# Performance work log

Hardware: AMD Instinct MI355X
Metric: run time of the kernel (lower is better)

Reference implementation:

```python
import jax, jax.numpy as jnp
import numpy as np

# MyConvT config (matches init_kwargs)
K, S, P, OP = 5, 2, 2, 1  # kernel, stride, padding, output_padding


def setup_inputs() -> dict:
    key = jax.random.key(0)
    k0, k1, k2, k3 = jax.random.split(key, 4)
    B, Cin, Cout, H, W = 8, 192, 128, 64, 64
    OH = (H - 1) * S + K - 2 * P + OP  # 128
    OW = (W - 1) * S + K - 2 * P + OP  # 128
    x = jax.random.normal(k0, (B, Cin, H, W), jnp.float32)
    # mask spatial must be (OH + K - 1, OW + K - 1) so its unfold has OH*OW columns
    mask = jax.random.randint(k1, (B, 1, OH + K - 1, OW + K - 1), 0, 2, jnp.int32)
    # torch ConvTranspose2d weight layout: [in_channels, out_channels, kH, kW]
    weight = jax.random.normal(k2, (Cin, Cout, K, K), jnp.float32) * 0.05
    bias = jax.random.normal(k3, (Cout,), jnp.float32) * 0.05
    return {"x": x, "mask": mask, "weight": weight, "bias": bias}


def _masked_conv_transpose(x, mask, weight, bias):
    # The torch module does: zero-insert (stride dilation), pad (K-1-P each side,
    # plus OP trailing), unfold, gather valid patches (where the unfolded mask
    # patch has any nonzero), dense matmul with rot180/transposed weight + bias,
    # then masked_scatter back (zeros elsewhere). Mathematically:
    #   out = mask_any * (conv_transpose2d(x, weight) + bias)
    # where mask_any[b,oh,ow] = any(mask[b,:, oh:oh+K, ow:ow+K] != 0).
    kern = jnp.flip(weight, (2, 3)).transpose(1, 0, 2, 3)  # -> OIHW correlation kernel
    pad = ((K - 1 - P, K - 1 - P + OP), (K - 1 - P, K - 1 - P + OP))
    y = jax.lax.conv_general_dilated(
        x, kern, window_strides=(1, 1), padding=pad, lhs_dilation=(S, S),
        dimension_numbers=("NCHW", "OIHW", "NCHW"))  # [B, Cout, OH, OW]
    m = (mask != 0).astype(y.dtype)  # [B, 1, OH+K-1, OW+K-1]
    pooled = jax.lax.reduce_window(m, 0.0, jax.lax.max,
                                   (1, 1, K, K), (1, 1, 1, 1), "VALID")  # [B,1,OH,OW]
    return jnp.where(pooled > 0, y + bias[None, :, None, None], 0.0)


def reference(x, mask, weight, bias):
    return _masked_conv_transpose(x, mask, weight, bias)
```

## Files before the change

kernel.cpp:

```cpp
#include <hip/hip_runtime.h>


#define NB   8
#define CIN  192
#define COUT 128
#define HH   64
#define OHH  128
#define OWW  128
#define MH   132
#define MW   132

#define X4_IYH_B 27648
#define PLANE_B  9216
#define XBUF_B   36864
#define WOFF     36864
#define NSLOT    5
#define LDS_B    (XBUF_B + NSLOT * 8192)

typedef short bf16x8 __attribute__((ext_vector_type(8)));
typedef float f32x4  __attribute__((ext_vector_type(4)));
typedef float f32x2  __attribute__((ext_vector_type(2)));

static __device__ __forceinline__ unsigned short f2bf(float f) {
  union { float f; unsigned int u; } a; a.f = f;
  return (unsigned short)((a.u + 0x7fffu + ((a.u >> 16) & 1u)) >> 16);
}

#define GLOAD_LDS16(gp, lp) __builtin_amdgcn_global_load_lds(                      \
    (const __attribute__((address_space(1))) void*)(gp),                           \
    (__attribute__((address_space(3))) void*)(lp), 16, 0, 0)

__global__ __launch_bounds__(256) void prep_k(
    const float* __restrict__ x, const int* __restrict__ mask,
    const float* __restrict__ w, unsigned short* __restrict__ x4,
    unsigned short* __restrict__ w4, unsigned char* __restrict__ many) {
  const int bid = blockIdx.x, tid = threadIdx.x;

  if (bid < 528) {
    const int b = bid / 66, iyH = bid % 66;
    const int lane = tid & 63, wv = tid >> 6;
    unsigned short* pl = x4 + (size_t)(b * 66 + iyH) * (X4_IYH_B / 2);

    if (iyH == 0 || iyH == 65) {
      for (int i = tid; i < X4_IYH_B / 16; i += 256)
        *(uint4*)(pl + i * 8) = make_uint4(0, 0, 0, 0);
      return;
    }
    const int iy = iyH - 1;
    if (tid < 48) {
      int c3 = tid >> 4, rr = (tid >> 3) & 1, ch = tid & 7;
      *(uint4*)(pl + (c3 * 72 + rr * 65) * 64 + ch * 8) = make_uint4(0, 0, 0, 0);
    }
    #pragma unroll
    for (int k = 0; k < 6; ++k) {
      int ci0 = wv * 48 + k * 8;
      int c3 = ci0 >> 6, cr = ci0 & 63;
      unsigned short p[8];
      #pragma unroll
      for (int e = 0; e < 8; ++e)
        p[e] = f2bf(x[(((size_t)b * CIN + ci0 + e) * HH + iy) * HH + lane]);
      uint4 v;
      v.x = (unsigned)p[0] | ((unsigned)p[1] << 16);
      v.y = (unsigned)p[2] | ((unsigned)p[3] << 16);
      v.z = (unsigned)p[4] | ((unsigned)p[5] << 16);
      v.w = (unsigned)p[6] | ((unsigned)p[7] << 16);
      *(uint4*)(pl + ((size_t)c3 * 72 + 1 + lane) * 64 + cr) = v;
    }
  } else if (bid < 624) {
    int idx = (bid - 528) * 256 + tid;
    int ci = idx % CIN, co = idx / CIN;
    int cob = co >> 6, c = co & 63, c3 = ci >> 6, cir = ci & 63;
    const float* src = w + (size_t)(ci * COUT + co) * 25;
    #pragma unroll
    for (int tap = 0; tap < 25; ++tap)
      w4[(size_t)((tap * 2 + cob) * 3 + c3) * 4096 + c * 64 + cir] = f2bf(src[tap]);
  } else {
    int g = (bid - 624) * 256 + tid;
    int owq = g & 31, oh = (g >> 5) & 127, b = g >> 12;
    const int* mp = mask + (b * MH + oh) * MW + owq * 4;
    int a0 = 0, a1 = 0, a2 = 0, a3 = 0;
    #pragma unroll
    for (int i = 0; i < 5; ++i) {
      int4 u = *(const int4*)(mp + i * MW);
      int4 v = *(const int4*)(mp + i * MW + 4);
      int c = u.z | u.w | v.x;
      a0 |= u.x | u.y | c;
      a1 |= u.y | c | v.y;
      a2 |= c | v.y | v.z;
      a3 |= u.w | v.x | v.y | v.z | v.w;
    }
    *(uchar4*)(many + ((size_t)b * OHH + oh) * OWW + owq * 4) =
        make_uchar4(a0 ? 1 : 0, a1 ? 1 : 0, a2 ? 1 : 0, a3 ? 1 : 0);
  }
}


#define VMC(N) asm volatile("s_waitcnt vmcnt(" #N ")" ::: "memory")

#define GATE(T)                                                                \
  { if ((T) == 24 && c3 == 2)      VMC(0);                                     \
    else if ((T) == 22 && c3 == 2) VMC(2);                                     \
    else                           VMC(6);                                     \
    __builtin_amdgcn_s_barrier(); }

#define BF_LOAD(KK, KJ)                                                        \
  { const int p_ = oyr + 2 - (KK);                                             \
    _Pragma("unroll") for (int k2 = 0; k2 < 2; ++k2)                           \
      _Pragma("unroll") for (int ti = 0; ti < 4; ++ti) {                       \
        const int row_ = ti * 16 + l15 + 2 - (KJ);                             \
        bfr[k2][ti] = *(const bf16x8*)(lds + p_ * PLANE_B + row_ * 128 +       \
                                       (((k2 * 4 + kc) ^ (row_ & 7)) << 4)); } }

#define AF_LOADJ(J, T)                                                         \
  { const char* ws_ = lds + WOFF + ((T) % 5) * 8192;                           \
    _Pragma("unroll") for (int k2 = 0; k2 < 2; ++k2)                           \
      _Pragma("unroll") for (int mi = 0; mi < 2; ++mi) {                       \
        const int row_ = cos * 32 + mi * 16 + l15;                             \
        afr[J][k2][mi] = *(const bf16x8*)(ws_ + row_ * 128 +                   \
                                          (((k2 * 4 + kc) ^ (l15 & 7)) << 4)); } }

#define MMJ(J, PH_, PW_)                                                       \
  { __builtin_amdgcn_s_setprio(1);                                             \
    _Pragma("unroll") for (int k2 = 0; k2 < 2; ++k2)                           \
      _Pragma("unroll") for (int mi = 0; mi < 2; ++mi)                         \
        _Pragma("unroll") for (int ti = 0; ti < 4; ++ti)                       \
          acc[PH_][PW_][mi][ti] = __builtin_amdgcn_mfma_f32_16x16x32_bf16(     \
              afr[J][k2][mi], bfr[k2][ti], acc[PH_][PW_][mi][ti], 0, 0, 0);    \
    __builtin_amdgcn_s_setprio(0); }

#define PAIRB(T, KK, KJ, PH0, PW0, PH1, PW1)                                   \
  { stage_u((T) + 3); stage_u((T) + 4); GATE(T)                                \
    BF_LOAD(KK, KJ) AF_LOADJ(0, T) AF_LOADJ(1, (T) + 1)                        \
    MMJ(0, PH0, PW0) MMJ(1, PH1, PW1) }
#define PAIRN(T, PH0, PW0, PH1, PW1)                                           \
  { stage_u((T) + 3); stage_u((T) + 4); GATE(T)                                \
    AF_LOADJ(0, T) AF_LOADJ(1, (T) + 1)                                        \
    MMJ(0, PH0, PW0) MMJ(1, PH1, PW1) }
#define PH1B(T, KK, KJ, PH0, PW0)                                              \
  { stage_u((T) + 3); GATE(T)                                                  \
    BF_LOAD(KK, KJ) AF_LOADJ(0, T) MMJ(0, PH0, PW0) }

__global__ __launch_bounds__(256, 2) void convt_mfma(
    const unsigned short* __restrict__ x4, const unsigned short* __restrict__ w4,
    const float* __restrict__ bias, const unsigned char* __restrict__ many,
    float* __restrict__ out) {
  __shared__ __align__(16) char lds[LDS_B];
  constexpr int TID[25] = {0,1,5,6, 2,3,7,8, 4,9, 10,11,15,16, 12,13,17,18,
                           14,19, 20,21, 22,23, 24};

  const int tid = threadIdx.x, lane = tid & 63, wv = tid >> 6;
  const int l15 = lane & 15, kc = lane >> 4;
  const int cos = wv & 1, oyr = wv >> 1;
  const int b = blockIdx.x & 7, qq = blockIdx.x >> 3;
  const int cob = qq & 1, oyq = qq >> 1;
  const int oy0 = oyq * 2, oy = oy0 + oyr;
  const int sswz = (lane >> 3) * 128 + (((lane & 7) ^ (lane >> 3)) << 4);

  const char* x4b = (const char*)x4 + (size_t)(b * 66 + oy0) * X4_IYH_B;
  const char* w4b = (const char*)w4 + cob * 24576;

  f32x4 acc[2][2][2][4];
  #pragma unroll
  for (int p = 0; p < 2; ++p)
    #pragma unroll
    for (int q2 = 0; q2 < 2; ++q2)
      #pragma unroll
      for (int i = 0; i < 2; ++i)
        #pragma unroll
        for (int j = 0; j < 4; ++j)
          acc[p][q2][i][j] = (f32x4){0.f, 0.f, 0.f, 0.f};

  auto stage_x = [&](int c3) {
    #pragma unroll
    for (int j = 0; j < 9; ++j) {
      int qc = wv + 4 * j;
      int p = qc / 9, ch = qc % 9;
      GLOAD_LDS16(x4b + (size_t)p * X4_IYH_B + c3 * PLANE_B + ch * 1024 + sswz,
                  lds + p * PLANE_B + ch * 1024 + lane * 16);
    }
  };
  auto stage_w = [&](int tapid, int c3n, int slot) {
    const char* s = w4b + (size_t)tapid * 49152 + c3n * 8192 + wv * 2048 + sswz;
    char* d = lds + WOFF + slot * 8192 + wv * 2048 + lane * 16;
    GLOAD_LDS16(s, d);
    GLOAD_LDS16(s + 1024, d + 1024);
  };
  int c3 = 0;
  auto stage_u = [&](int u) {
    if (u <= 24) stage_w(TID[u], c3, u % 5);
    else if (c3 < 2) stage_w(TID[u - 25], c3 + 1, (u - 25) % 5);
  };

  stage_x(0);
  stage_w(TID[0], 0, 0);
  stage_w(TID[1], 0, 1);
  stage_w(TID[2], 0, 2);

  bf16x8 bfr[2][4], afr[2][2][2];
  #pragma unroll 1
  for (c3 = 0; c3 < 3; ++c3) {
    PAIRB(0,  0, 0,  0, 0,  0, 1)
    PAIRN(2,         1, 0,  1, 1)
    PAIRB(4,  0, 1,  0, 0,  0, 1)
    PAIRN(6,         1, 0,  1, 1)
    PAIRB(8,  0, 2,  0, 0,  1, 0)
    PAIRB(10, 1, 0,  0, 0,  0, 1)
    PAIRN(12,        1, 0,  1, 1)
    PAIRB(14, 1, 1,  0, 0,  0, 1)
    PAIRN(16,        1, 0,  1, 1)
    PAIRB(18, 1, 2,  0, 0,  1, 0)
    PAIRB(20, 2, 0,  0, 0,  0, 1)
    PAIRB(22, 2, 1,  0, 0,  0, 1)
    PH1B (24, 2, 2,  0, 0)
    if (c3 < 2) {
      __builtin_amdgcn_s_barrier();
      stage_x(c3 + 1);
      VMC(0);
      __builtin_amdgcn_s_barrier();
    }
  }

  const int cobase = cob * 64 + cos * 32;
  #pragma unroll
  for (int mi = 0; mi < 2; ++mi) {
    const f32x4 bv = *(const f32x4*)(bias + cobase + mi * 16 + kc * 4);
    #pragma unroll
    for (int ph = 0; ph < 2; ++ph) {
      const int oh = 2 * oy + ph;
      const unsigned char* mrow = many + ((size_t)b * OHH + oh) * OWW;
      #pragma unroll
      for (int ti = 0; ti < 4; ++ti) {
        const int ow0 = 2 * (ti * 16 + l15);
        const unsigned short m2 = *(const unsigned short*)(mrow + ow0);
        #pragma unroll
        for (int r = 0; r < 4; ++r) {
          const int co = cobase + mi * 16 + kc * 4 + r;
          f32x2 v;
          v.x = (m2 & 0x00FFu) ? acc[ph][0][mi][ti][r] + bv[r] : 0.f;
          v.y = (m2 & 0xFF00u) ? acc[ph][1][mi][ti][r] + bv[r] : 0.f;
          *(f32x2*)(out + (((size_t)(b * COUT + co)) * OHH + oh) * OWW + ow0) = v;
        }
      }
    }
  }
}

extern "C" void kernel_launch(void* const* d_in, const int* in_sizes, int n_in,
                              void* d_out, int out_size, void* d_ws, size_t ws_size,
                              hipStream_t stream) {
  const float* x    = (const float*)d_in[0];
  const int*   mask = (const int*)d_in[1];
  const float* w    = (const float*)d_in[2];
  const float* bias = (const float*)d_in[3];
  float* out = (float*)d_out;

  unsigned char*  many = (unsigned char*)d_ws;
  unsigned short* x4   = (unsigned short*)((char*)d_ws + 131072);
  unsigned short* w4   = (unsigned short*)((char*)d_ws + 131072 +
                                           (size_t)NB * 66 * X4_IYH_B);

  prep_k<<<752, 256, 0, stream>>>(x, mask, w, x4, w4, many);
  convt_mfma<<<512, 256, 0, stream>>>(x4, w4, bias, many, out);
}
```

Measured before the change: 55.12 us.

## Split x-plane staging to overlap next chunk's input load with final taps

```diff
diff --git a/kernel.cpp b/kernel.cpp
--- a/kernel.cpp
+++ b/kernel.cpp
@@ -97,12 +97,6 @@
 
 #define VMC(N) asm volatile("s_waitcnt vmcnt(" #N ")" ::: "memory")
 
-#define GATE(T)                                                                \
-  { if ((T) == 24 && c3 == 2)      VMC(0);                                     \
-    else if ((T) == 22 && c3 == 2) VMC(2);                                     \
-    else                           VMC(6);                                     \
-    __builtin_amdgcn_s_barrier(); }
-
 #define BF_LOAD(KK, KJ)                                                        \
   { const int p_ = oyr + 2 - (KK);                                             \
     _Pragma("unroll") for (int k2 = 0; k2 < 2; ++k2)                           \
@@ -129,15 +123,31 @@
     __builtin_amdgcn_s_setprio(0); }
 
 #define PAIRB(T, KK, KJ, PH0, PW0, PH1, PW1)                                   \
-  { stage_u((T) + 3); stage_u((T) + 4); GATE(T)                                \
+  { stage_u((T) + 3); stage_u((T) + 4); VMC(6);                                \
+    __builtin_amdgcn_s_barrier();                                              \
     BF_LOAD(KK, KJ) AF_LOADJ(0, T) AF_LOADJ(1, (T) + 1)                        \
     MMJ(0, PH0, PW0) MMJ(1, PH1, PW1) }
 #define PAIRN(T, PH0, PW0, PH1, PW1)                                           \
-  { stage_u((T) + 3); stage_u((T) + 4); GATE(T)                                \
+  { stage_u((T) + 3); stage_u((T) + 4); VMC(6);                                \
+    __builtin_amdgcn_s_barrier();                                              \
     AF_LOADJ(0, T) AF_LOADJ(1, (T) + 1)                                        \
     MMJ(0, PH0, PW0) MMJ(1, PH1, PW1) }
-#define PH1B(T, KK, KJ, PH0, PW0)                                              \
-  { stage_u((T) + 3); GATE(T)                                                  \
+#define PAIR0(T, KK, KJ, PH0, PW0, PH1, PW1)                                   \
+  { stage_u((T) + 3); stage_u((T) + 4);                                        \
+    if (c3 == 0) { VMC(6); } else { VMC(10); }                                 \
+    __builtin_amdgcn_s_barrier();                                              \
+    BF_LOAD(KK, KJ) AF_LOADJ(0, T) AF_LOADJ(1, (T) + 1)                        \
+    MMJ(0, PH0, PW0) MMJ(1, PH1, PW1) }
+#define PAIRX(T, KK, KJ, PH0, PW0, PH1, PW1)                                   \
+  { stage_u((T) + 3); stage_u((T) + 4);                                        \
+    if (c3 < 2) { stage_xr(c3 + 1, 18, 36); VMC(10); } else { VMC(2); }        \
+    __builtin_amdgcn_s_barrier();                                              \
+    BF_LOAD(KK, KJ) AF_LOADJ(0, T) AF_LOADJ(1, (T) + 1)                        \
+    MMJ(0, PH0, PW0) MMJ(1, PH1, PW1) }
+#define PH1BX(T, KK, KJ, PH0, PW0)                                             \
+  { stage_u((T) + 3);                                                          \
+    if (c3 < 2) { VMC(10); } else { VMC(0); }                                  \
+    __builtin_amdgcn_s_barrier();                                              \
     BF_LOAD(KK, KJ) AF_LOADJ(0, T) MMJ(0, PH0, PW0) }
 
 __global__ __launch_bounds__(256, 2) void convt_mfma(
@@ -170,12 +180,10 @@
         for (int j = 0; j < 4; ++j)
           acc[p][q2][i][j] = (f32x4){0.f, 0.f, 0.f, 0.f};
 
-  auto stage_x = [&](int c3) {
-    #pragma unroll
-    for (int j = 0; j < 9; ++j) {
-      int qc = wv + 4 * j;
+  auto stage_xr = [&](int c3n, int qlo, int qhi) {
+    for (int qc = qlo + wv; qc < qhi; qc += 4) {
       int p = qc / 9, ch = qc % 9;
-      GLOAD_LDS16(x4b + (size_t)p * X4_IYH_B + c3 * PLANE_B + ch * 1024 + sswz,
+      GLOAD_LDS16(x4b + (size_t)p * X4_IYH_B + c3n * PLANE_B + ch * 1024 + sswz,
                   lds + p * PLANE_B + ch * 1024 + lane * 16);
     }
   };
@@ -191,7 +199,7 @@
     else if (c3 < 2) stage_w(TID[u - 25], c3 + 1, (u - 25) % 5);
   };
 
-  stage_x(0);
+  stage_xr(0, 0, 36);
   stage_w(TID[0], 0, 0);
   stage_w(TID[1], 0, 1);
   stage_w(TID[2], 0, 2);
@@ -199,7 +207,7 @@
   bf16x8 bfr[2][4], afr[2][2][2];
   #pragma unroll 1
   for (c3 = 0; c3 < 3; ++c3) {
-    PAIRB(0,  0, 0,  0, 0,  0, 1)
+    PAIR0(0,  0, 0,  0, 0,  0, 1)
     PAIRN(2,         1, 0,  1, 1)
     PAIRB(4,  0, 1,  0, 0,  0, 1)
     PAIRN(6,         1, 0,  1, 1)
@@ -210,13 +218,11 @@
     PAIRN(16,        1, 0,  1, 1)
     PAIRB(18, 1, 2,  0, 0,  1, 0)
     PAIRB(20, 2, 0,  0, 0,  0, 1)
-    PAIRB(22, 2, 1,  0, 0,  0, 1)
-    PH1B (24, 2, 2,  0, 0)
+    PAIRX(22, 2, 1,  0, 0,  0, 1)
+    PH1BX(24, 2, 2,  0, 0)
     if (c3 < 2) {
       __builtin_amdgcn_s_barrier();
-      stage_x(c3 + 1);
-      VMC(0);
-      __builtin_amdgcn_s_barrier();
+      stage_xr(c3 + 1, 0, 18);
     }
   }
 
```

Result: slower. 59.79 us (+8.5%).
